# Performance work log

Hardware: AMD Instinct MI355X
Metric: run time of the kernel (lower is better)

Reference implementation:

```python
import jax, jax.numpy as jnp
import numpy as np


def setup_inputs() -> dict:
    key = jax.random.key(0)
    kf, kx1, ky1, kw, kh = jax.random.split(key, 5)
    B, H, W, C, R = 4, 64, 64, 256, 128
    feature_map = jax.random.normal(kf, (B, H, W, C), dtype=jnp.float32)
    # valid boxes [x1,y1,x2,y2] with side lengths in [8,32] (>= 7x7 grid -> no empty bins)
    x1 = jax.random.uniform(kx1, (B, R), minval=0.0, maxval=W - 33.0)
    y1 = jax.random.uniform(ky1, (B, R), minval=0.0, maxval=H - 33.0)
    bw = jax.random.uniform(kw, (B, R), minval=8.0, maxval=32.0)
    bh = jax.random.uniform(kh, (B, R), minval=8.0, maxval=32.0)
    rois = jnp.stack([x1, y1, x1 + bw, y1 + bh], axis=-1)
    return {"feature_map": feature_map, "rois": rois, "pooling_h": 7, "pooling_w": 7}


def _bin_bounds(start, end, n):
    # start/end: int32 [B] absolute coords; returns (lo, hi) int32 [B, n] per-bin bounds.
    # Mirrors TF: float steps truncated to int32 (floor for nonneg); last bin ends at roi size.
    size = (end - start).astype(jnp.float32)            # [B]
    step = size / n
    k = jnp.arange(n, dtype=jnp.float32)                # [n]
    lo_rel = (k[None, :] * step[:, None]).astype(jnp.int32)
    hi_rel = jnp.where(jnp.arange(n)[None, :] + 1 < n,
                       ((k[None, :] + 1.0) * step[:, None]).astype(jnp.int32),
                       (end - start)[:, None])
    return start[:, None] + lo_rel, start[:, None] + hi_rel


def _roi_pool(feature_map, rois, ph, pw):
    B, H, W, C = feature_map.shape
    neg = jnp.array(-jnp.inf, feature_map.dtype)
    hidx = jnp.arange(H)
    widx = jnp.arange(W)

    def per_roi(carry, roi):  # roi: [B, 4] = [x1, y1, x2, y2]
        ws = jnp.maximum(jnp.round(roi[:, 0]).astype(jnp.int32), 0)
        hs = jnp.maximum(jnp.round(roi[:, 1]).astype(jnp.int32), 0)
        we = jnp.minimum(jnp.round(roi[:, 2]).astype(jnp.int32), W)
        he = jnp.minimum(jnp.round(roi[:, 3]).astype(jnp.int32), H)
        hlo, hhi = _bin_bounds(hs, he, ph)   # [B, ph]
        wlo, whi = _bin_bounds(ws, we, pw)   # [B, pw]
        mh = (hidx[None, None, :] >= hlo[:, :, None]) & (hidx[None, None, :] < hhi[:, :, None])  # [B,ph,H]
        mw = (widx[None, None, :] >= wlo[:, :, None]) & (widx[None, None, :] < whi[:, :, None])  # [B,pw,W]
        # masked max over w per w-bin, then over h per h-bin (bins partition the ROI)
        colmax = jnp.where(mw[:, :, None, :, None], feature_map[:, None], neg).max(axis=3)  # [B,pw,H,C]
        pooled = jnp.where(mh[:, :, None, :, None], colmax[:, None], neg).max(axis=3)       # [B,ph,pw,C]
        # TF code enumerates bins j-outer/i-inner but reshapes to (ph,pw): replicate that quirk.
        out = jnp.swapaxes(pooled, 1, 2).reshape(B, ph, pw, C)
        return carry, out

    _, outs = jax.lax.scan(per_roi, None, jnp.swapaxes(rois, 0, 1))  # [R,B,ph,pw,C]
    return jnp.swapaxes(outs, 0, 1)  # [B,R,ph,pw,C]


def reference(feature_map, rois, pooling_h, pooling_w):
    return _roi_pool(feature_map, rois, pooling_h, pooling_w)
```

## Files before the change

kernel.cpp:

```cpp
#include <hip/hip_runtime.h>
#include <math.h>

#define B 4
#define H 64
#define W 64
#define C 256
#define R 128
#define PH 7
#define PW 7

#define CELLS_TOTAL (B * R * PH * PW)
#define BLOCKS_TOTAL (CELLS_TOTAL / 4)
#define BLOCKS_PER_HALF 784

typedef float f32x4 __attribute__((ext_vector_type(4)));

__global__ __launch_bounds__(256) void roi_pool_kernel(
    const float* __restrict__ fm,
    const float* __restrict__ rois,
    float* __restrict__ out)
{
    const int wave = threadIdx.x >> 6;
    const int lane = threadIdx.x & 63;

    const int xcd  = blockIdx.x & 7;
    const int slot = blockIdx.x >> 3;
    const int b    = xcd >> 1;
    const int half = xcd & 1;
    const int cell_in_b = (half * BLOCKS_PER_HALF + slot) * 4 + wave;

    const int q = cell_in_b % PW;
    int t = cell_in_b / PW;
    const int p = t % PH;
    const int r = t / PH;

    const int ridx = __builtin_amdgcn_readfirstlane(b * R + r);
    const float* roi = rois + (size_t)ridx * 4;
    const float x1 = roi[0], y1 = roi[1], x2 = roi[2], y2 = roi[3];

    int ws = max((int)rintf(x1), 0);
    int hs = max((int)rintf(y1), 0);
    int we = min((int)rintf(x2), W);
    int he = min((int)rintf(y2), H);

    const float hstep = (float)(he - hs) / 7.0f;
    const float wstep = (float)(we - ws) / 7.0f;
    const int hlo = hs + (int)((float)q * hstep);
    const int hhi = (q < PH - 1) ? (hs + (int)((float)(q + 1) * hstep)) : he;
    const int wlo = ws + (int)((float)p * wstep);
    const int whi = (p < PW - 1) ? (ws + (int)((float)(p + 1) * wstep)) : we;

    const int nw = whi - wlo;
    const int nh = hhi - hlo;
    const int n  = nh * nw;

    const float* gp = fm + ((size_t)(b * H + hlo) * W + wlo) * C + lane * 4;
    int gw = 0;
    const size_t rstep = (size_t)(W - nw + 1) * C;

    f32x4 acc = { -INFINITY, -INFINITY, -INFINITY, -INFINITY };

#define LOADV(dst) (dst) = *(const f32x4*)gp
#define ADV() { if (++gw == nw) { gw = 0; gp += rstep; } else { gp += (size_t)C; } }
#define FM(vv) { acc.x = fmaxf(acc.x, (vv).x); acc.y = fmaxf(acc.y, (vv).y); \
                 acc.z = fmaxf(acc.z, (vv).z); acc.w = fmaxf(acc.w, (vv).w); }

    if (n >= 8) {
        f32x4 v0, v1, v2, v3, v4, v5, v6, v7;
        LOADV(v0); ADV(); LOADV(v1); ADV(); LOADV(v2); ADV(); LOADV(v3); ADV();
        LOADV(v4); ADV(); LOADV(v5); ADV(); LOADV(v6); ADV(); LOADV(v7); ADV();
        int k = n - 8;
        while (k >= 8) {
            FM(v0); LOADV(v0); ADV();
            FM(v1); LOADV(v1); ADV();
            FM(v2); LOADV(v2); ADV();
            FM(v3); LOADV(v3); ADV();
            FM(v4); LOADV(v4); ADV();
            FM(v5); LOADV(v5); ADV();
            FM(v6); LOADV(v6); ADV();
            FM(v7); LOADV(v7); ADV();
            k -= 8;
        }
        if (k > 0) { FM(v0); LOADV(v0); ADV(); }
        if (k > 1) { FM(v1); LOADV(v1); ADV(); }
        if (k > 2) { FM(v2); LOADV(v2); ADV(); }
        if (k > 3) { FM(v3); LOADV(v3); ADV(); }
        if (k > 4) { FM(v4); LOADV(v4); ADV(); }
        if (k > 5) { FM(v5); LOADV(v5); ADV(); }
        if (k > 6) { FM(v6); LOADV(v6); ADV(); }
        FM(v0); FM(v1); FM(v2); FM(v3); FM(v4); FM(v5); FM(v6); FM(v7);
    } else if (n >= 4) {
        f32x4 v0, v1, v2, v3;
        LOADV(v0); ADV(); LOADV(v1); ADV(); LOADV(v2); ADV(); LOADV(v3); ADV();
        int k = n - 4;
        if (k > 0) { FM(v0); LOADV(v0); ADV(); }
        if (k > 1) { FM(v1); LOADV(v1); ADV(); }
        if (k > 2) { FM(v2); LOADV(v2); ADV(); }
        FM(v0); FM(v1); FM(v2); FM(v3);
    } else {
        for (int i = 0; i < n; ++i) {
            f32x4 v; LOADV(v); ADV(); FM(v);
        }
    }

    const int cell = ((b * R + r) * PH + p) * PW + q;
    float* op = out + (size_t)cell * C + lane * 4;
    __builtin_nontemporal_store(acc, (f32x4*)op);
}

extern "C" void kernel_launch(void* const* d_in, const int* in_sizes, int n_in,
                              void* d_out, int out_size, void* d_ws, size_t ws_size,
                              hipStream_t stream) {
    const float* fm   = (const float*)d_in[0];
    const float* rois = (const float*)d_in[1];
    float* out = (float*)d_out;

    roi_pool_kernel<<<BLOCKS_TOTAL, 256, 0, stream>>>(fm, rois, out);
}
```

Before: 15.63 us.

## Split each wave across two pooling cells with channel halves per XCD pair

Each wave now processes two adjacent output cells, one per 32-lane half, and each block covers only half of the 256 channels, chosen by the XCD parity. Trip counts use the max element count of the two cells, and lanes with fewer elements stop advancing their pointer, so they reload their last element, which leaves the max unchanged. The aim is to let more cells run concurrently and to balance work. The cost is duplicated index math, loads that are repeated or divergent, and trip counts sized to the larger cell.

```diff
diff --git a/kernel.cpp b/kernel.cpp
--- a/kernel.cpp
+++ b/kernel.cpp
@@ -9,9 +9,8 @@
 #define PH 7
 #define PW 7
 
-#define CELLS_TOTAL (B * R * PH * PW)
-#define BLOCKS_TOTAL (CELLS_TOTAL / 4)
-#define BLOCKS_PER_HALF 784
+#define BLOCKS_TOTAL 6272
+#define PAIRS_PER_BATCH 3136
 
 typedef float f32x4 __attribute__((ext_vector_type(4)));
 
@@ -22,21 +21,24 @@
 {
     const int wave = threadIdx.x >> 6;
     const int lane = threadIdx.x & 63;
+    const int half = lane >> 5;
+    const int l    = lane & 31;
 
-    const int xcd  = blockIdx.x & 7;
-    const int slot = blockIdx.x >> 3;
-    const int b    = xcd >> 1;
-    const int half = xcd & 1;
-    const int cell_in_b = (half * BLOCKS_PER_HALF + slot) * 4 + wave;
+    const int xcd   = blockIdx.x & 7;
+    const int slot  = blockIdx.x >> 3;
+    const int b     = xcd >> 1;
+    const int chalf = xcd & 1;
+
+    const int pair = slot * 4 + wave;
+    const int cell_in_b = pair * 2 + half;
 
     const int q = cell_in_b % PW;
     int t = cell_in_b / PW;
     const int p = t % PH;
     const int r = t / PH;
 
-    const int ridx = __builtin_amdgcn_readfirstlane(b * R + r);
-    const float* roi = rois + (size_t)ridx * 4;
-    const float x1 = roi[0], y1 = roi[1], x2 = roi[2], y2 = roi[3];
+    const f32x4 roi = *(const f32x4*)(rois + (size_t)(b * R + r) * 4);
+    const float x1 = roi.x, y1 = roi.y, x2 = roi.z, y2 = roi.w;
 
     int ws = max((int)rintf(x1), 0);
     int hs = max((int)rintf(y1), 0);
@@ -54,22 +56,28 @@
     const int nh = hhi - hlo;
     const int n  = nh * nw;
 
-    const float* gp = fm + ((size_t)(b * H + hlo) * W + wlo) * C + lane * 4;
+    const int nmax = max(__builtin_amdgcn_readlane(n, 0),
+                         __builtin_amdgcn_readlane(n, 32));
+
+    const int cbase = chalf * 128 + l * 4;
+    const float* gp = fm + ((size_t)(b * H + hlo) * W + wlo) * C + cbase;
     int gw = 0;
+    int left = n;
     const size_t rstep = (size_t)(W - nw + 1) * C;
 
     f32x4 acc = { -INFINITY, -INFINITY, -INFINITY, -INFINITY };
 
 #define LOADV(dst) (dst) = *(const f32x4*)gp
-#define ADV() { if (++gw == nw) { gw = 0; gp += rstep; } else { gp += (size_t)C; } }
+#define ADV() { if (left > 1) { --left; \
+                  if (++gw == nw) { gw = 0; gp += rstep; } else { gp += (size_t)C; } } }
 #define FM(vv) { acc.x = fmaxf(acc.x, (vv).x); acc.y = fmaxf(acc.y, (vv).y); \
                  acc.z = fmaxf(acc.z, (vv).z); acc.w = fmaxf(acc.w, (vv).w); }
 
-    if (n >= 8) {
+    if (nmax >= 8) {
         f32x4 v0, v1, v2, v3, v4, v5, v6, v7;
         LOADV(v0); ADV(); LOADV(v1); ADV(); LOADV(v2); ADV(); LOADV(v3); ADV();
         LOADV(v4); ADV(); LOADV(v5); ADV(); LOADV(v6); ADV(); LOADV(v7); ADV();
-        int k = n - 8;
+        int k = nmax - 8;
         while (k >= 8) {
             FM(v0); LOADV(v0); ADV();
             FM(v1); LOADV(v1); ADV();
@@ -89,22 +97,22 @@
         if (k > 5) { FM(v5); LOADV(v5); ADV(); }
         if (k > 6) { FM(v6); LOADV(v6); ADV(); }
         FM(v0); FM(v1); FM(v2); FM(v3); FM(v4); FM(v5); FM(v6); FM(v7);
-    } else if (n >= 4) {
+    } else if (nmax >= 4) {
         f32x4 v0, v1, v2, v3;
         LOADV(v0); ADV(); LOADV(v1); ADV(); LOADV(v2); ADV(); LOADV(v3); ADV();
-        int k = n - 4;
+        int k = nmax - 4;
         if (k > 0) { FM(v0); LOADV(v0); ADV(); }
         if (k > 1) { FM(v1); LOADV(v1); ADV(); }
         if (k > 2) { FM(v2); LOADV(v2); ADV(); }
         FM(v0); FM(v1); FM(v2); FM(v3);
     } else {
-        for (int i = 0; i < n; ++i) {
+        for (int i = 0; i < nmax; ++i) {
             f32x4 v; LOADV(v); ADV(); FM(v);
         }
     }
 
     const int cell = ((b * R + r) * PH + p) * PW + q;
-    float* op = out + (size_t)cell * C + lane * 4;
+    float* op = out + (size_t)cell * C + cbase;
     __builtin_nontemporal_store(acc, (f32x4*)op);
 }
 
```

Result: slower. 16.37 us (+4.7%).

## Split channels across XCD pairs instead of splitting cells

Applied to the files above, without the earlier changes.

Each wave now covers half the channel range (128 channels, 2 floats per lane) for every cell of its batch, rather than all 256 channels for half the cells. The two XCDs that share a batch split the channels, so each XCD's L2 only holds half of that batch's feature-map channels, which should cut footprint and improve cache reuse. The cost is twice as many blocks doing half the work each, with 8-byte loads in place of 16-byte loads, so per-block ROI setup overhead is doubled.

```diff
diff --git a/kernel.cpp b/kernel.cpp
--- a/kernel.cpp
+++ b/kernel.cpp
@@ -9,11 +9,11 @@
 #define PH 7
 #define PW 7
 
-#define CELLS_TOTAL (B * R * PH * PW)
-#define BLOCKS_TOTAL (CELLS_TOTAL / 4)
-#define BLOCKS_PER_HALF 784
+#define CELLS_PER_BATCH (R * PH * PW)
+#define BLOCKS_PER_CLASS (CELLS_PER_BATCH / 4)
+#define BLOCKS_TOTAL (BLOCKS_PER_CLASS * 8)
 
-typedef float f32x4 __attribute__((ext_vector_type(4)));
+typedef float f32x2 __attribute__((ext_vector_type(2)));
 
 __global__ __launch_bounds__(256) void roi_pool_kernel(
     const float* __restrict__ fm,
@@ -23,11 +23,12 @@
     const int wave = threadIdx.x >> 6;
     const int lane = threadIdx.x & 63;
 
-    const int xcd  = blockIdx.x & 7;
-    const int slot = blockIdx.x >> 3;
-    const int b    = xcd >> 1;
-    const int half = xcd & 1;
-    const int cell_in_b = (half * BLOCKS_PER_HALF + slot) * 4 + wave;
+    const int xcd   = blockIdx.x & 7;
+    const int slot  = blockIdx.x >> 3;
+    const int b     = xcd >> 1;
+    const int chalf = xcd & 1;
+
+    const int cell_in_b = slot * 4 + wave;
 
     const int q = cell_in_b % PW;
     int t = cell_in_b / PW;
@@ -54,19 +55,19 @@
     const int nh = hhi - hlo;
     const int n  = nh * nw;
 
-    const float* gp = fm + ((size_t)(b * H + hlo) * W + wlo) * C + lane * 4;
+    const int cbase = chalf * 128 + lane * 2;
+    const float* gp = fm + ((size_t)(b * H + hlo) * W + wlo) * C + cbase;
     int gw = 0;
     const size_t rstep = (size_t)(W - nw + 1) * C;
 
-    f32x4 acc = { -INFINITY, -INFINITY, -INFINITY, -INFINITY };
+    f32x2 acc = { -INFINITY, -INFINITY };
 
-#define LOADV(dst) (dst) = *(const f32x4*)gp
+#define LOADV(dst) (dst) = *(const f32x2*)gp
 #define ADV() { if (++gw == nw) { gw = 0; gp += rstep; } else { gp += (size_t)C; } }
-#define FM(vv) { acc.x = fmaxf(acc.x, (vv).x); acc.y = fmaxf(acc.y, (vv).y); \
-                 acc.z = fmaxf(acc.z, (vv).z); acc.w = fmaxf(acc.w, (vv).w); }
+#define FM(vv) { acc.x = fmaxf(acc.x, (vv).x); acc.y = fmaxf(acc.y, (vv).y); }
 
     if (n >= 8) {
-        f32x4 v0, v1, v2, v3, v4, v5, v6, v7;
+        f32x2 v0, v1, v2, v3, v4, v5, v6, v7;
         LOADV(v0); ADV(); LOADV(v1); ADV(); LOADV(v2); ADV(); LOADV(v3); ADV();
         LOADV(v4); ADV(); LOADV(v5); ADV(); LOADV(v6); ADV(); LOADV(v7); ADV();
         int k = n - 8;
@@ -90,7 +91,7 @@
         if (k > 6) { FM(v6); LOADV(v6); ADV(); }
         FM(v0); FM(v1); FM(v2); FM(v3); FM(v4); FM(v5); FM(v6); FM(v7);
     } else if (n >= 4) {
-        f32x4 v0, v1, v2, v3;
+        f32x2 v0, v1, v2, v3;
         LOADV(v0); ADV(); LOADV(v1); ADV(); LOADV(v2); ADV(); LOADV(v3); ADV();
         int k = n - 4;
         if (k > 0) { FM(v0); LOADV(v0); ADV(); }
@@ -99,13 +100,13 @@
         FM(v0); FM(v1); FM(v2); FM(v3);
     } else {
         for (int i = 0; i < n; ++i) {
-            f32x4 v; LOADV(v); ADV(); FM(v);
+            f32x2 v; LOADV(v); ADV(); FM(v);
         }
     }
 
     const int cell = ((b * R + r) * PH + p) * PW + q;
-    float* op = out + (size_t)cell * C + lane * 4;
-    __builtin_nontemporal_store(acc, (f32x4*)op);
+    float* op = out + (size_t)cell * C + cbase;
+    __builtin_nontemporal_store(acc, (f32x2*)op);
 }
 
 extern "C" void kernel_launch(void* const* d_in, const int* in_sizes, int n_in,
```

New measurement: 21.79 us. 1.39x slower.
